# Optimization experiments

Measured on AMD Instinct MI355X. Metric: run time of the kernel, lower is better.

The kernel has to match this reference:

```python
import jax, jax.numpy as jnp
import numpy as np

N = 8192
IN_DIM = 256
HIDDEN = 128


def setup_inputs() -> dict:
    key = jax.random.key(0)
    k1, k2 = jax.random.split(key)
    X = jax.random.normal(k1, (N, IN_DIM), dtype=jnp.float32)
    # nn.Linear(in_dim, hidden, bias=False): weight [hidden, in_dim]
    W = jax.random.normal(k2, (HIDDEN, IN_DIM), dtype=jnp.float32) * (1.0 / np.sqrt(IN_DIM))
    return {"X": X, "W": W}


def reference(X, W):
    # Z = X @ W.T : [N, hidden]
    Z = jnp.einsum('ni,hi->nh', X, W)
    # Dense similarity graph: ReLU(Z Z^T), row-normalized
    A = jax.nn.relu(jnp.einsum('nh,mh->nm', Z, Z))  # [N, N]
    A = A / (A.sum(axis=-1, keepdims=True) + 1e-6)
    out = jnp.einsum('nm,mh->nh', A, Z)  # [N, hidden]
    return (out, A)
```

## Files before the change

### kernel.cpp

```cpp
#include <hip/hip_runtime.h>


#define NR 8192
#define KD 256
#define HD 128

typedef short v8s __attribute__((ext_vector_type(8)));
typedef float v4f __attribute__((ext_vector_type(4)));

static __device__ __forceinline__ ushort f2bf(float f) {
    union { float f; unsigned u; } c; c.f = f;
    unsigned u = c.u;
    u += 0x7fffu + ((u >> 16) & 1u);
    return (ushort)(u >> 16);
}
static __device__ __forceinline__ float bf2f(ushort b) {
    union { unsigned u; float f; } c; c.u = ((unsigned)b) << 16; return c.f;
}
static __device__ __forceinline__ unsigned pk2(float a, float b) {
    union { float f; unsigned u; } x, y; x.f = a; y.f = b;
    unsigned ua = x.u + 0x7fffu + ((x.u >> 16) & 1u);
    unsigned ub = y.u + 0x7fffu + ((y.u >> 16) & 1u);
    return (ua >> 16) | (ub & 0xffff0000u);
}

__global__ __launch_bounds__(256) void k_z(const float* __restrict__ X,
                                           const float* __restrict__ W,
                                           ushort* __restrict__ Zb,
                                           ushort* __restrict__ ZbT) {
    __shared__ ushort Xhi[32][264];
    __shared__ ushort Xlo[32][264];
    int tid = threadIdx.x, lane = tid & 63, wave = tid >> 6;
    int lm = lane & 15, lq = lane >> 4;
    int n0 = blockIdx.x * 32;
    int hbase = wave * 32;
    v8s Whi[2][8], Wlo[2][8];
#pragma unroll
    for (int hi = 0; hi < 2; ++hi) {
        const float* wp = W + (hbase + hi * 16 + lm) * KD + lq * 8;
#pragma unroll
        for (int ks = 0; ks < 8; ++ks) {
            float4 w0 = *(const float4*)(wp + ks * 32);
            float4 w1 = *(const float4*)(wp + ks * 32 + 4);
            float wv[8] = {w0.x, w0.y, w0.z, w0.w, w1.x, w1.y, w1.z, w1.w};
#pragma unroll
            for (int j = 0; j < 8; ++j) {
                ushort h = f2bf(wv[j]);
                Whi[hi][ks][j] = (short)h;
                Wlo[hi][ks][j] = (short)f2bf(wv[j] - bf2f(h));
            }
        }
    }
#pragma unroll
    for (int t = 0; t < 8; ++t) {
        int idx = tid + t * 256;
        int r = idx >> 6, c4 = (idx & 63) * 4;
        float4 x = *(const float4*)(X + (size_t)(n0 + r) * KD + c4);
        ushort h0 = f2bf(x.x), h1 = f2bf(x.y), h2 = f2bf(x.z), h3 = f2bf(x.w);
        unsigned a = ((unsigned)h0) | ((unsigned)h1 << 16);
        unsigned b = ((unsigned)h2) | ((unsigned)h3 << 16);
        unsigned c = ((unsigned)f2bf(x.x - bf2f(h0))) | ((unsigned)f2bf(x.y - bf2f(h1)) << 16);
        unsigned d = ((unsigned)f2bf(x.z - bf2f(h2))) | ((unsigned)f2bf(x.w - bf2f(h3)) << 16);
        *(uint2*)&Xhi[r][c4] = make_uint2(a, b);
        *(uint2*)&Xlo[r][c4] = make_uint2(c, d);
    }
    __syncthreads();
#pragma unroll
    for (int ni = 0; ni < 2; ++ni) {
        v8s Ah[8], Al[8];
#pragma unroll
        for (int ks = 0; ks < 8; ++ks) {
            Ah[ks] = *(const v8s*)&Xhi[ni * 16 + lm][ks * 32 + lq * 8];
            Al[ks] = *(const v8s*)&Xlo[ni * 16 + lm][ks * 32 + lq * 8];
        }
        v4f acc[2] = {{0.f, 0.f, 0.f, 0.f}, {0.f, 0.f, 0.f, 0.f}};
#pragma unroll
        for (int ks = 0; ks < 8; ++ks)
#pragma unroll
            for (int hi = 0; hi < 2; ++hi) {
                acc[hi] = __builtin_amdgcn_mfma_f32_16x16x32_bf16(Ah[ks], Whi[hi][ks], acc[hi], 0, 0, 0);
                acc[hi] = __builtin_amdgcn_mfma_f32_16x16x32_bf16(Ah[ks], Wlo[hi][ks], acc[hi], 0, 0, 0);
                acc[hi] = __builtin_amdgcn_mfma_f32_16x16x32_bf16(Al[ks], Whi[hi][ks], acc[hi], 0, 0, 0);
            }
#pragma unroll
        for (int hi = 0; hi < 2; ++hi) {
            int h = hbase + hi * 16 + lm;
            int nb = n0 + ni * 16 + lq * 4;
            ushort b0 = f2bf(acc[hi][0]), b1 = f2bf(acc[hi][1]);
            ushort b2 = f2bf(acc[hi][2]), b3 = f2bf(acc[hi][3]);
            Zb[(size_t)(nb + 0) * HD + h] = b0;
            Zb[(size_t)(nb + 1) * HD + h] = b1;
            Zb[(size_t)(nb + 2) * HD + h] = b2;
            Zb[(size_t)(nb + 3) * HD + h] = b3;
            *(uint2*)&ZbT[(size_t)h * NR + nb] =
                make_uint2(((unsigned)b0) | ((unsigned)b1 << 16), ((unsigned)b2) | ((unsigned)b3 << 16));
        }
    }
}

__global__ __launch_bounds__(256) void k_rowsum(const ushort* __restrict__ Zb,
                                                float* __restrict__ rowsum) {
    __shared__ ushort ZR[128][136];
    __shared__ ushort ZC[128][136];
    int tid = threadIdx.x, lane = tid & 63, wave = tid >> 6;
    int lm = lane & 15, lq = lane >> 4;
    int rb = blockIdx.x >> 3, cs = blockIdx.x & 7;
    int row0 = rb * 128, cstart = cs * 1024;
#pragma unroll
    for (int t = 0; t < 8; ++t) {
        int idx = tid + t * 256;
        int r = idx >> 4, c8 = (idx & 15) * 8;
        *(uint4*)&ZR[r][c8] = *(const uint4*)(Zb + (size_t)(row0 + r) * HD + c8);
    }
    __syncthreads();
    int wr2 = wave >> 1, wc2 = wave & 1;
    v8s Bfr[4][4];
#pragma unroll
    for (int ri = 0; ri < 4; ++ri)
#pragma unroll
        for (int ks = 0; ks < 4; ++ks)
            Bfr[ri][ks] = *(const v8s*)&ZR[wr2 * 64 + ri * 16 + lm][ks * 32 + lq * 8];
    float rs[4] = {0.f, 0.f, 0.f, 0.f};
    for (int it = 0; it < 8; ++it) {
        int c0 = cstart + it * 128;
        __syncthreads();
#pragma unroll
        for (int t = 0; t < 8; ++t) {
            int idx = tid + t * 256;
            int r = idx >> 4, c8 = (idx & 15) * 8;
            *(uint4*)&ZC[r][c8] = *(const uint4*)(Zb + (size_t)(c0 + r) * HD + c8);
        }
        __syncthreads();
#pragma unroll
        for (int ci = 0; ci < 4; ++ci) {
            v8s Af[4];
#pragma unroll
            for (int ks = 0; ks < 4; ++ks)
                Af[ks] = *(const v8s*)&ZC[wc2 * 64 + ci * 16 + lm][ks * 32 + lq * 8];
            v4f acc[4] = {{0.f,0.f,0.f,0.f},{0.f,0.f,0.f,0.f},{0.f,0.f,0.f,0.f},{0.f,0.f,0.f,0.f}};
#pragma unroll
            for (int ks = 0; ks < 4; ++ks)
#pragma unroll
                for (int ri = 0; ri < 4; ++ri)
                    acc[ri] = __builtin_amdgcn_mfma_f32_16x16x32_bf16(Af[ks], Bfr[ri][ks], acc[ri], 0, 0, 0);
#pragma unroll
            for (int ri = 0; ri < 4; ++ri)
                rs[ri] += fmaxf(acc[ri][0], 0.f) + fmaxf(acc[ri][1], 0.f) +
                          fmaxf(acc[ri][2], 0.f) + fmaxf(acc[ri][3], 0.f);
        }
    }
#pragma unroll
    for (int ri = 0; ri < 4; ++ri) {
        float v = rs[ri];
        v += __shfl_xor(v, 16, 64);
        v += __shfl_xor(v, 32, 64);
        if (lq == 0) atomicAdd(&rowsum[row0 + wr2 * 64 + ri * 16 + lm], v);
    }
}

__global__ __launch_bounds__(256) void k_main(const ushort* __restrict__ Zb,
                                              const ushort* __restrict__ ZbT,
                                              const float* __restrict__ rowsum,
                                              float* __restrict__ outp,
                                              float* __restrict__ Ap) {
    __shared__ ushort ZR[64][136];
    __shared__ ushort ZC[64][136];
    __shared__ ushort ZCT[128][72];
    __shared__ ushort PT[64][72];
    int tid = threadIdx.x, lane = tid & 63, wave = tid >> 6;
    int lm = lane & 15, lq = lane >> 4;
    int rb = blockIdx.x >> 2, cs = blockIdx.x & 3;
    int row0 = rb * 64, colb = cs * 2048;
#pragma unroll
    for (int t = 0; t < 4; ++t) {
        int idx = tid + t * 256;
        int r = idx >> 4, c8 = (idx & 15) * 8;
        *(uint4*)&ZR[r][c8] = *(const uint4*)(Zb + (size_t)(row0 + r) * HD + c8);
    }
    __syncthreads();
    int wr2 = wave >> 1, wc2 = wave & 1;
    v8s Bfr[2][4];
#pragma unroll
    for (int ri = 0; ri < 2; ++ri)
#pragma unroll
        for (int ks = 0; ks < 4; ++ks)
            Bfr[ri][ks] = *(const v8s*)&ZR[wr2 * 32 + ri * 16 + lm][ks * 32 + lq * 8];
    float rsv[2];
#pragma unroll
    for (int ri = 0; ri < 2; ++ri)
        rsv[ri] = 1.0f / (rowsum[row0 + wr2 * 32 + ri * 16 + lm] + 1e-6f);
    v4f U[2][4];
#pragma unroll
    for (int ri = 0; ri < 2; ++ri)
#pragma unroll
        for (int hi = 0; hi < 4; ++hi) U[ri][hi] = (v4f){0.f, 0.f, 0.f, 0.f};

    for (int it = 0; it < 32; ++it) {
        int c0 = colb + it * 64;
        __syncthreads();
#pragma unroll
        for (int t = 0; t < 4; ++t) {
            int idx = tid + t * 256;
            int r = idx >> 4, c8 = (idx & 15) * 8;
            *(uint4*)&ZC[r][c8] = *(const uint4*)(Zb + (size_t)(c0 + r) * HD + c8);
        }
#pragma unroll
        for (int t = 0; t < 4; ++t) {
            int idx = tid + t * 256;
            int hh = idx >> 3, cc8 = (idx & 7) * 8;
            *(uint4*)&ZCT[hh][cc8] = *(const uint4*)(ZbT + (size_t)hh * NR + c0 + cc8);
        }
        __syncthreads();
#pragma unroll
        for (int ci = 0; ci < 2; ++ci) {
            v8s Af[4];
#pragma unroll
            for (int ks = 0; ks < 4; ++ks)
                Af[ks] = *(const v8s*)&ZC[wc2 * 32 + ci * 16 + lm][ks * 32 + lq * 8];
            v4f S0 = {0.f, 0.f, 0.f, 0.f}, S1 = {0.f, 0.f, 0.f, 0.f};
#pragma unroll
            for (int ks = 0; ks < 4; ++ks) {
                S0 = __builtin_amdgcn_mfma_f32_16x16x32_bf16(Af[ks], Bfr[0][ks], S0, 0, 0, 0);
                S1 = __builtin_amdgcn_mfma_f32_16x16x32_bf16(Af[ks], Bfr[1][ks], S1, 0, 0, 0);
            }
            int cb = wc2 * 32 + ci * 16 + lq * 4;
            {
                int r = wr2 * 32 + lm;
                v4f av;
                av[0] = fmaxf(S0[0], 0.f) * rsv[0]; av[1] = fmaxf(S0[1], 0.f) * rsv[0];
                av[2] = fmaxf(S0[2], 0.f) * rsv[0]; av[3] = fmaxf(S0[3], 0.f) * rsv[0];
                __builtin_nontemporal_store(av, (v4f*)(Ap + (size_t)(row0 + r) * NR + c0 + cb));
                *(uint2*)&PT[r][cb] = make_uint2(pk2(av[0], av[1]), pk2(av[2], av[3]));
            }
            {
                int r = wr2 * 32 + 16 + lm;
                v4f av;
                av[0] = fmaxf(S1[0], 0.f) * rsv[1]; av[1] = fmaxf(S1[1], 0.f) * rsv[1];
                av[2] = fmaxf(S1[2], 0.f) * rsv[1]; av[3] = fmaxf(S1[3], 0.f) * rsv[1];
                __builtin_nontemporal_store(av, (v4f*)(Ap + (size_t)(row0 + r) * NR + c0 + cb));
                *(uint2*)&PT[r][cb] = make_uint2(pk2(av[0], av[1]), pk2(av[2], av[3]));
            }
        }
        __syncthreads();
#pragma unroll
        for (int ks = 0; ks < 2; ++ks) {
            v8s P0 = *(const v8s*)&PT[wr2 * 32 + lm][ks * 32 + lq * 8];
            v8s P1 = *(const v8s*)&PT[wr2 * 32 + 16 + lm][ks * 32 + lq * 8];
#pragma unroll
            for (int hi = 0; hi < 4; ++hi) {
                v8s Bz = *(const v8s*)&ZCT[wc2 * 64 + hi * 16 + lm][ks * 32 + lq * 8];
                U[0][hi] = __builtin_amdgcn_mfma_f32_16x16x32_bf16(P0, Bz, U[0][hi], 0, 0, 0);
                U[1][hi] = __builtin_amdgcn_mfma_f32_16x16x32_bf16(P1, Bz, U[1][hi], 0, 0, 0);
            }
        }
    }
#pragma unroll
    for (int ri = 0; ri < 2; ++ri)
#pragma unroll
        for (int hi = 0; hi < 4; ++hi)
#pragma unroll
            for (int j = 0; j < 4; ++j)
                atomicAdd(&outp[(size_t)(row0 + wr2 * 32 + ri * 16 + lq * 4 + j) * HD +
                                wc2 * 64 + hi * 16 + lm],
                          U[ri][hi][j]);
}

extern "C" void kernel_launch(void* const* d_in, const int* in_sizes, int n_in,
                              void* d_out, int out_size, void* d_ws, size_t ws_size,
                              hipStream_t stream) {
    (void)in_sizes; (void)n_in; (void)out_size; (void)ws_size;
    const float* X = (const float*)d_in[0];
    const float* W = (const float*)d_in[1];
    float* outp = (float*)d_out;
    float* Ap = outp + (size_t)NR * HD;
    char* ws = (char*)d_ws;
    ushort* Zb = (ushort*)ws;
    ushort* ZbT = (ushort*)(ws + (size_t)NR * HD * 2);
    float* rowsum = (float*)(ws + (size_t)NR * HD * 4);

    (void)hipMemsetAsync(outp, 0, (size_t)NR * HD * sizeof(float), stream);
    (void)hipMemsetAsync(rowsum, 0, NR * sizeof(float), stream);
    k_z<<<dim3(NR / 32), dim3(256), 0, stream>>>(X, W, Zb, ZbT);
    k_rowsum<<<dim3(512), dim3(256), 0, stream>>>(Zb, rowsum);
    k_main<<<dim3(512), dim3(256), 0, stream>>>(Zb, ZbT, rowsum, outp, Ap);
}
```

Before: 367.1 us.

## Compute unnormalized ReLU(ZZ^T)·Z in rowsum pass, normalize output afterward

The P·Z product is moved out of the A-writing kernel and into the rowsum kernel. It accumulates the unnormalized relu(S)·Z there, and a small final kernel scales the result by the reciprocal row sum. This leaves the A-writing kernel doing only the score GEMM and streaming stores, which may raise its occupancy (launch_bounds 256,4). The cost is more LDS and register pressure in the rowsum kernel (launch_bounds 256,1), an extra workspace buffer with a memset and a pass over it, and bf16 rounding of unnormalized values instead of normalized ones.

```diff
diff --git a/kernel.cpp b/kernel.cpp
--- a/kernel.cpp
+++ b/kernel.cpp
@@ -98,10 +98,14 @@
     }
 }
 
-__global__ __launch_bounds__(256) void k_rowsum(const ushort* __restrict__ Zb,
-                                                float* __restrict__ rowsum) {
+__global__ __launch_bounds__(256, 1) void k_sv(const ushort* __restrict__ Zb,
+                                               const ushort* __restrict__ ZbT,
+                                               float* __restrict__ rowsum,
+                                               float* __restrict__ Vacc) {
     __shared__ ushort ZR[128][136];
     __shared__ ushort ZC[128][136];
+    __shared__ ushort ZCT[128][136];
+    __shared__ ushort PT[128][136];
     int tid = threadIdx.x, lane = tid & 63, wave = tid >> 6;
     int lm = lane & 15, lq = lane >> 4;
     int rb = blockIdx.x >> 3, cs = blockIdx.x & 7;
@@ -121,6 +125,12 @@
         for (int ks = 0; ks < 4; ++ks)
             Bfr[ri][ks] = *(const v8s*)&ZR[wr2 * 64 + ri * 16 + lm][ks * 32 + lq * 8];
     float rs[4] = {0.f, 0.f, 0.f, 0.f};
+    v4f V[4][4];
+#pragma unroll
+    for (int ri = 0; ri < 4; ++ri)
+#pragma unroll
+        for (int hi = 0; hi < 4; ++hi) V[ri][hi] = (v4f){0.f, 0.f, 0.f, 0.f};
+
     for (int it = 0; it < 8; ++it) {
         int c0 = cstart + it * 128;
         __syncthreads();
@@ -130,6 +140,12 @@
             int r = idx >> 4, c8 = (idx & 15) * 8;
             *(uint4*)&ZC[r][c8] = *(const uint4*)(Zb + (size_t)(c0 + r) * HD + c8);
         }
+#pragma unroll
+        for (int t = 0; t < 8; ++t) {
+            int idx = tid + t * 256;
+            int h = idx >> 4, cc8 = (idx & 15) * 8;
+            *(uint4*)&ZCT[h][cc8] = *(const uint4*)(ZbT + (size_t)h * NR + c0 + cc8);
+        }
         __syncthreads();
 #pragma unroll
         for (int ci = 0; ci < 4; ++ci) {
@@ -144,9 +160,28 @@
                 for (int ri = 0; ri < 4; ++ri)
                     acc[ri] = __builtin_amdgcn_mfma_f32_16x16x32_bf16(Af[ks], Bfr[ri][ks], acc[ri], 0, 0, 0);
 #pragma unroll
+            for (int ri = 0; ri < 4; ++ri) {
+                float a0 = fmaxf(acc[ri][0], 0.f), a1 = fmaxf(acc[ri][1], 0.f);
+                float a2 = fmaxf(acc[ri][2], 0.f), a3 = fmaxf(acc[ri][3], 0.f);
+                rs[ri] += a0 + a1 + a2 + a3;
+                *(uint2*)&PT[wr2 * 64 + ri * 16 + lm][wc2 * 64 + ci * 16 + lq * 4] =
+                    make_uint2(pk2(a0, a1), pk2(a2, a3));
+            }
+        }
+        __syncthreads();
+#pragma unroll
+        for (int ks = 0; ks < 4; ++ks) {
+            v8s Pf[4];
+#pragma unroll
             for (int ri = 0; ri < 4; ++ri)
-                rs[ri] += fmaxf(acc[ri][0], 0.f) + fmaxf(acc[ri][1], 0.f) +
-                          fmaxf(acc[ri][2], 0.f) + fmaxf(acc[ri][3], 0.f);
+                Pf[ri] = *(const v8s*)&PT[wr2 * 64 + ri * 16 + lm][ks * 32 + lq * 8];
+#pragma unroll
+            for (int hi = 0; hi < 4; ++hi) {
+                v8s Bz = *(const v8s*)&ZCT[wc2 * 64 + hi * 16 + lm][ks * 32 + lq * 8];
+#pragma unroll
+                for (int ri = 0; ri < 4; ++ri)
+                    V[ri][hi] = __builtin_amdgcn_mfma_f32_16x16x32_bf16(Pf[ri], Bz, V[ri][hi], 0, 0, 0);
+            }
         }
     }
 #pragma unroll
@@ -156,17 +191,22 @@
         v += __shfl_xor(v, 32, 64);
         if (lq == 0) atomicAdd(&rowsum[row0 + wr2 * 64 + ri * 16 + lm], v);
     }
-}
-
-__global__ __launch_bounds__(256) void k_main(const ushort* __restrict__ Zb,
-                                              const ushort* __restrict__ ZbT,
+#pragma unroll
+    for (int ri = 0; ri < 4; ++ri)
+#pragma unroll
+        for (int hi = 0; hi < 4; ++hi)
+#pragma unroll
+            for (int j = 0; j < 4; ++j)
+                atomicAdd(&Vacc[(size_t)(row0 + wr2 * 64 + ri * 16 + lq * 4 + j) * HD +
+                                wc2 * 64 + hi * 16 + lm],
+                          V[ri][hi][j]);
+}
+
+__global__ __launch_bounds__(256, 4) void k_a(const ushort* __restrict__ Zb,
                                               const float* __restrict__ rowsum,
-                                              float* __restrict__ outp,
                                               float* __restrict__ Ap) {
     __shared__ ushort ZR[64][136];
     __shared__ ushort ZC[64][136];
-    __shared__ ushort ZCT[128][72];
-    __shared__ ushort PT[64][72];
     int tid = threadIdx.x, lane = tid & 63, wave = tid >> 6;
     int lm = lane & 15, lq = lane >> 4;
     int rb = blockIdx.x >> 2, cs = blockIdx.x & 3;
@@ -189,11 +229,6 @@
 #pragma unroll
     for (int ri = 0; ri < 2; ++ri)
         rsv[ri] = 1.0f / (rowsum[row0 + wr2 * 32 + ri * 16 + lm] + 1e-6f);
-    v4f U[2][4];
-#pragma unroll
-    for (int ri = 0; ri < 2; ++ri)
-#pragma unroll
-        for (int hi = 0; hi < 4; ++hi) U[ri][hi] = (v4f){0.f, 0.f, 0.f, 0.f};
 
     for (int it = 0; it < 32; ++it) {
         int c0 = colb + it * 64;
@@ -203,12 +238,6 @@
             int idx = tid + t * 256;
             int r = idx >> 4, c8 = (idx & 15) * 8;
             *(uint4*)&ZC[r][c8] = *(const uint4*)(Zb + (size_t)(c0 + r) * HD + c8);
-        }
-#pragma unroll
-        for (int t = 0; t < 4; ++t) {
-            int idx = tid + t * 256;
-            int hh = idx >> 3, cc8 = (idx & 7) * 8;
-            *(uint4*)&ZCT[hh][cc8] = *(const uint4*)(ZbT + (size_t)hh * NR + c0 + cc8);
         }
         __syncthreads();
 #pragma unroll
@@ -230,7 +259,6 @@
                 av[0] = fmaxf(S0[0], 0.f) * rsv[0]; av[1] = fmaxf(S0[1], 0.f) * rsv[0];
                 av[2] = fmaxf(S0[2], 0.f) * rsv[0]; av[3] = fmaxf(S0[3], 0.f) * rsv[0];
                 __builtin_nontemporal_store(av, (v4f*)(Ap + (size_t)(row0 + r) * NR + c0 + cb));
-                *(uint2*)&PT[r][cb] = make_uint2(pk2(av[0], av[1]), pk2(av[2], av[3]));
             }
             {
                 int r = wr2 * 32 + 16 + lm;
@@ -238,31 +266,20 @@
                 av[0] = fmaxf(S1[0], 0.f) * rsv[1]; av[1] = fmaxf(S1[1], 0.f) * rsv[1];
                 av[2] = fmaxf(S1[2], 0.f) * rsv[1]; av[3] = fmaxf(S1[3], 0.f) * rsv[1];
                 __builtin_nontemporal_store(av, (v4f*)(Ap + (size_t)(row0 + r) * NR + c0 + cb));
-                *(uint2*)&PT[r][cb] = make_uint2(pk2(av[0], av[1]), pk2(av[2], av[3]));
-            }
-        }
-        __syncthreads();
-#pragma unroll
-        for (int ks = 0; ks < 2; ++ks) {
-            v8s P0 = *(const v8s*)&PT[wr2 * 32 + lm][ks * 32 + lq * 8];
-            v8s P1 = *(const v8s*)&PT[wr2 * 32 + 16 + lm][ks * 32 + lq * 8];
-#pragma unroll
-            for (int hi = 0; hi < 4; ++hi) {
-                v8s Bz = *(const v8s*)&ZCT[wc2 * 64 + hi * 16 + lm][ks * 32 + lq * 8];
-                U[0][hi] = __builtin_amdgcn_mfma_f32_16x16x32_bf16(P0, Bz, U[0][hi], 0, 0, 0);
-                U[1][hi] = __builtin_amdgcn_mfma_f32_16x16x32_bf16(P1, Bz, U[1][hi], 0, 0, 0);
-            }
-        }
-    }
-#pragma unroll
-    for (int ri = 0; ri < 2; ++ri)
-#pragma unroll
-        for (int hi = 0; hi < 4; ++hi)
-#pragma unroll
-            for (int j = 0; j < 4; ++j)
-                atomicAdd(&outp[(size_t)(row0 + wr2 * 32 + ri * 16 + lq * 4 + j) * HD +
-                                wc2 * 64 + hi * 16 + lm],
-                          U[ri][hi][j]);
+            }
+        }
+    }
+}
+
+__global__ __launch_bounds__(256) void k_out(const float* __restrict__ Vacc,
+                                             const float* __restrict__ rowsum,
+                                             float* __restrict__ outp) {
+    int idx = blockIdx.x * 256 + threadIdx.x;
+    int r = idx >> 5, h4 = (idx & 31) * 4;
+    float rsv = 1.0f / (rowsum[r] + 1e-6f);
+    float4 v = *(const float4*)(Vacc + (size_t)r * HD + h4);
+    float4 o = make_float4(v.x * rsv, v.y * rsv, v.z * rsv, v.w * rsv);
+    *(float4*)(outp + (size_t)r * HD + h4) = o;
 }
 
 extern "C" void kernel_launch(void* const* d_in, const int* in_sizes, int n_in,
@@ -277,10 +294,12 @@
     ushort* Zb = (ushort*)ws;
     ushort* ZbT = (ushort*)(ws + (size_t)NR * HD * 2);
     float* rowsum = (float*)(ws + (size_t)NR * HD * 4);
-
-    (void)hipMemsetAsync(outp, 0, (size_t)NR * HD * sizeof(float), stream);
+    float* Vacc = (float*)(ws + (size_t)NR * HD * 4 + NR * 4);
+
     (void)hipMemsetAsync(rowsum, 0, NR * sizeof(float), stream);
+    (void)hipMemsetAsync(Vacc, 0, (size_t)NR * HD * sizeof(float), stream);
     k_z<<<dim3(NR / 32), dim3(256), 0, stream>>>(X, W, Zb, ZbT);
-    k_rowsum<<<dim3(512), dim3(256), 0, stream>>>(Zb, rowsum);
-    k_main<<<dim3(512), dim3(256), 0, stream>>>(Zb, ZbT, rowsum, outp, Ap);
-}
+    k_sv<<<dim3(512), dim3(256), 0, stream>>>(Zb, ZbT, rowsum, Vacc);
+    k_a<<<dim3(512), dim3(256), 0, stream>>>(Zb, rowsum, Ap);
+    k_out<<<dim3(1024), dim3(256), 0, stream>>>(Vacc, rowsum, outp);
+}
```

New measurement: 446.6 us. 1.22x slower.

## Fuse rowsum with unnormalized A·Z, then write normalized A separately

Applied to the files above, without the earlier changes.

The work is restructured so one kernel computes the row sums and the unnormalized product relu(ZZ^T)·Z together, using split-column partials instead of atomics. A small kernel reduces the partials and applies the normalization to produce the output. A final kernel writes A straight from global/L2 loads without LDS staging, and the P operand now uses the hardware bf16 pack instruction. The partial V buffers are staged in the tail of the A output region, which is overwritten afterwards. This removes the memsets and atomics but computes ZZ^T twice and feeds the PV matmul with unnormalized bf16 values.

```diff
diff --git a/kernel.cpp b/kernel.cpp
--- a/kernel.cpp
+++ b/kernel.cpp
@@ -17,11 +17,10 @@
 static __device__ __forceinline__ float bf2f(ushort b) {
     union { unsigned u; float f; } c; c.u = ((unsigned)b) << 16; return c.f;
 }
-static __device__ __forceinline__ unsigned pk2(float a, float b) {
-    union { float f; unsigned u; } x, y; x.f = a; y.f = b;
-    unsigned ua = x.u + 0x7fffu + ((x.u >> 16) & 1u);
-    unsigned ub = y.u + 0x7fffu + ((y.u >> 16) & 1u);
-    return (ua >> 16) | (ub & 0xffff0000u);
+static __device__ __forceinline__ unsigned cvtpk(float a, float b) {
+    unsigned r;
+    asm("v_cvt_pk_bf16_f32 %0, %1, %2" : "=v"(r) : "v"(a), "v"(b));
+    return r;
 }
 
 __global__ __launch_bounds__(256) void k_z(const float* __restrict__ X,
@@ -98,171 +97,165 @@
     }
 }
 
-__global__ __launch_bounds__(256) void k_rowsum(const ushort* __restrict__ Zb,
-                                                float* __restrict__ rowsum) {
-    __shared__ ushort ZR[128][136];
-    __shared__ ushort ZC[128][136];
+__global__ __launch_bounds__(256) void k_sv(const ushort* __restrict__ Zb,
+                                            const ushort* __restrict__ ZbT,
+                                            float* __restrict__ rsP,
+                                            float* __restrict__ Vp) {
+    __shared__ ushort PT[2][32][136];
+    __shared__ float rsred[4][32];
     int tid = threadIdx.x, lane = tid & 63, wave = tid >> 6;
     int lm = lane & 15, lq = lane >> 4;
-    int rb = blockIdx.x >> 3, cs = blockIdx.x & 7;
-    int row0 = rb * 128, cstart = cs * 1024;
-#pragma unroll
-    for (int t = 0; t < 8; ++t) {
-        int idx = tid + t * 256;
-        int r = idx >> 4, c8 = (idx & 15) * 8;
-        *(uint4*)&ZR[r][c8] = *(const uint4*)(Zb + (size_t)(row0 + r) * HD + c8);
-    }
-    __syncthreads();
-    int wr2 = wave >> 1, wc2 = wave & 1;
-    v8s Bfr[4][4];
-#pragma unroll
-    for (int ri = 0; ri < 4; ++ri)
+    int rb = blockIdx.x >> 2, q = blockIdx.x & 3;
+    int row0 = rb * 32, cbase = q * 2048;
+    v8s Bfr[2][4];
+#pragma unroll
+    for (int ri = 0; ri < 2; ++ri)
 #pragma unroll
         for (int ks = 0; ks < 4; ++ks)
-            Bfr[ri][ks] = *(const v8s*)&ZR[wr2 * 64 + ri * 16 + lm][ks * 32 + lq * 8];
-    float rs[4] = {0.f, 0.f, 0.f, 0.f};
-    for (int it = 0; it < 8; ++it) {
-        int c0 = cstart + it * 128;
+            Bfr[ri][ks] = *(const v8s*)(Zb + (size_t)(row0 + ri * 16 + lm) * HD + ks * 32 + lq * 8);
+    float rs[2] = {0.f, 0.f};
+    v4f V[2][2];
+#pragma unroll
+    for (int ri = 0; ri < 2; ++ri)
+#pragma unroll
+        for (int hi = 0; hi < 2; ++hi) V[ri][hi] = (v4f){0.f, 0.f, 0.f, 0.f};
+
+    const ushort* afp = Zb + (size_t)(cbase + wave * 32 + lm) * HD + lq * 8;
+    const ushort* bzp = ZbT + (size_t)(wave * 32 + lm) * NR + cbase + lq * 8;
+
+    for (int it = 0; it < 16; ++it) {
+        v8s Bz[2][4];
+#pragma unroll
+        for (int hi = 0; hi < 2; ++hi)
+#pragma unroll
+            for (int ks = 0; ks < 4; ++ks)
+                Bz[hi][ks] = *(const v8s*)(bzp + (size_t)hi * 16 * NR + ks * 32);
+#pragma unroll
+        for (int ci = 0; ci < 2; ++ci) {
+            v8s Af[4];
+#pragma unroll
+            for (int ks = 0; ks < 4; ++ks)
+                Af[ks] = *(const v8s*)(afp + (size_t)(ci * 16) * HD + ks * 32);
+            v4f a0 = {0.f, 0.f, 0.f, 0.f}, a1 = {0.f, 0.f, 0.f, 0.f};
+#pragma unroll
+            for (int ks = 0; ks < 4; ++ks) {
+                a0 = __builtin_amdgcn_mfma_f32_16x16x32_bf16(Af[ks], Bfr[0][ks], a0, 0, 0, 0);
+                a1 = __builtin_amdgcn_mfma_f32_16x16x32_bf16(Af[ks], Bfr[1][ks], a1, 0, 0, 0);
+            }
+            int cc = wave * 32 + ci * 16 + lq * 4;
+            {
+                float f0 = fmaxf(a0[0], 0.f), f1 = fmaxf(a0[1], 0.f);
+                float f2 = fmaxf(a0[2], 0.f), f3 = fmaxf(a0[3], 0.f);
+                rs[0] += f0 + f1 + f2 + f3;
+                *(uint2*)&PT[it & 1][lm][cc] = make_uint2(cvtpk(f0, f1), cvtpk(f2, f3));
+            }
+            {
+                float f0 = fmaxf(a1[0], 0.f), f1 = fmaxf(a1[1], 0.f);
+                float f2 = fmaxf(a1[2], 0.f), f3 = fmaxf(a1[3], 0.f);
+                rs[1] += f0 + f1 + f2 + f3;
+                *(uint2*)&PT[it & 1][16 + lm][cc] = make_uint2(cvtpk(f0, f1), cvtpk(f2, f3));
+            }
+        }
         __syncthreads();
 #pragma unroll
-        for (int t = 0; t < 8; ++t) {
-            int idx = tid + t * 256;
-            int r = idx >> 4, c8 = (idx & 15) * 8;
-            *(uint4*)&ZC[r][c8] = *(const uint4*)(Zb + (size_t)(c0 + r) * HD + c8);
-        }
-        __syncthreads();
-#pragma unroll
-        for (int ci = 0; ci < 4; ++ci) {
-            v8s Af[4];
-#pragma unroll
-            for (int ks = 0; ks < 4; ++ks)
-                Af[ks] = *(const v8s*)&ZC[wc2 * 64 + ci * 16 + lm][ks * 32 + lq * 8];
-            v4f acc[4] = {{0.f,0.f,0.f,0.f},{0.f,0.f,0.f,0.f},{0.f,0.f,0.f,0.f},{0.f,0.f,0.f,0.f}};
-#pragma unroll
-            for (int ks = 0; ks < 4; ++ks)
-#pragma unroll
-                for (int ri = 0; ri < 4; ++ri)
-                    acc[ri] = __builtin_amdgcn_mfma_f32_16x16x32_bf16(Af[ks], Bfr[ri][ks], acc[ri], 0, 0, 0);
-#pragma unroll
-            for (int ri = 0; ri < 4; ++ri)
-                rs[ri] += fmaxf(acc[ri][0], 0.f) + fmaxf(acc[ri][1], 0.f) +
-                          fmaxf(acc[ri][2], 0.f) + fmaxf(acc[ri][3], 0.f);
-        }
-    }
-#pragma unroll
-    for (int ri = 0; ri < 4; ++ri) {
+        for (int ks = 0; ks < 4; ++ks) {
+            v8s P0 = *(const v8s*)&PT[it & 1][lm][ks * 32 + lq * 8];
+            v8s P1 = *(const v8s*)&PT[it & 1][16 + lm][ks * 32 + lq * 8];
+#pragma unroll
+            for (int hi = 0; hi < 2; ++hi) {
+                V[0][hi] = __builtin_amdgcn_mfma_f32_16x16x32_bf16(P0, Bz[hi][ks], V[0][hi], 0, 0, 0);
+                V[1][hi] = __builtin_amdgcn_mfma_f32_16x16x32_bf16(P1, Bz[hi][ks], V[1][hi], 0, 0, 0);
+            }
+        }
+        afp += (size_t)128 * HD;
+        bzp += 128;
+    }
+#pragma unroll
+    for (int ri = 0; ri < 2; ++ri) {
         float v = rs[ri];
         v += __shfl_xor(v, 16, 64);
         v += __shfl_xor(v, 32, 64);
-        if (lq == 0) atomicAdd(&rowsum[row0 + wr2 * 64 + ri * 16 + lm], v);
-    }
-}
-
-__global__ __launch_bounds__(256) void k_main(const ushort* __restrict__ Zb,
-                                              const ushort* __restrict__ ZbT,
-                                              const float* __restrict__ rowsum,
-                                              float* __restrict__ outp,
-                                              float* __restrict__ Ap) {
-    __shared__ ushort ZR[64][136];
-    __shared__ ushort ZC[64][136];
-    __shared__ ushort ZCT[128][72];
-    __shared__ ushort PT[64][72];
+        if (lq == 0) rsred[wave][ri * 16 + lm] = v;
+    }
+    __syncthreads();
+    if (tid < 32)
+        rsP[(size_t)q * NR + row0 + tid] =
+            rsred[0][tid] + rsred[1][tid] + rsred[2][tid] + rsred[3][tid];
+    float* vbase = Vp + (size_t)q * NR * HD + (size_t)row0 * HD + wave * 32;
+#pragma unroll
+    for (int ri = 0; ri < 2; ++ri)
+#pragma unroll
+        for (int hi = 0; hi < 2; ++hi)
+#pragma unroll
+            for (int j = 0; j < 4; ++j)
+                vbase[(size_t)(ri * 16 + lq * 4 + j) * HD + hi * 16 + lm] = V[ri][hi][j];
+}
+
+__global__ __launch_bounds__(256) void k_out(const float* __restrict__ Vp,
+                                             const float* __restrict__ rsP,
+                                             float* __restrict__ outp) {
+    int idx = blockIdx.x * 256 + threadIdx.x;
+    int r = idx >> 5, h4 = (idx & 31) * 4;
+    float rsv = 1.0f / (rsP[r] + rsP[NR + r] + rsP[2 * NR + r] + rsP[3 * NR + r] + 1e-6f);
+    size_t o = (size_t)r * HD + h4;
+    float4 v0 = *(const float4*)(Vp + o);
+    float4 v1 = *(const float4*)(Vp + (size_t)NR * HD + o);
+    float4 v2 = *(const float4*)(Vp + 2 * (size_t)NR * HD + o);
+    float4 v3 = *(const float4*)(Vp + 3 * (size_t)NR * HD + o);
+    float4 s = make_float4((v0.x + v1.x + v2.x + v3.x) * rsv, (v0.y + v1.y + v2.y + v3.y) * rsv,
+                           (v0.z + v1.z + v2.z + v3.z) * rsv, (v0.w + v1.w + v2.w + v3.w) * rsv);
+    *(float4*)(outp + o) = s;
+}
+
+__global__ __launch_bounds__(256) void k_a(const ushort* __restrict__ Zb,
+                                           const float* __restrict__ rsP,
+                                           float* __restrict__ Ap) {
     int tid = threadIdx.x, lane = tid & 63, wave = tid >> 6;
     int lm = lane & 15, lq = lane >> 4;
     int rb = blockIdx.x >> 2, cs = blockIdx.x & 3;
     int row0 = rb * 64, colb = cs * 2048;
-#pragma unroll
-    for (int t = 0; t < 4; ++t) {
-        int idx = tid + t * 256;
-        int r = idx >> 4, c8 = (idx & 15) * 8;
-        *(uint4*)&ZR[r][c8] = *(const uint4*)(Zb + (size_t)(row0 + r) * HD + c8);
-    }
-    __syncthreads();
     int wr2 = wave >> 1, wc2 = wave & 1;
     v8s Bfr[2][4];
 #pragma unroll
     for (int ri = 0; ri < 2; ++ri)
 #pragma unroll
         for (int ks = 0; ks < 4; ++ks)
-            Bfr[ri][ks] = *(const v8s*)&ZR[wr2 * 32 + ri * 16 + lm][ks * 32 + lq * 8];
+            Bfr[ri][ks] =
+                *(const v8s*)(Zb + (size_t)(row0 + wr2 * 32 + ri * 16 + lm) * HD + ks * 32 + lq * 8);
     float rsv[2];
 #pragma unroll
-    for (int ri = 0; ri < 2; ++ri)
-        rsv[ri] = 1.0f / (rowsum[row0 + wr2 * 32 + ri * 16 + lm] + 1e-6f);
-    v4f U[2][4];
-#pragma unroll
-    for (int ri = 0; ri < 2; ++ri)
-#pragma unroll
-        for (int hi = 0; hi < 4; ++hi) U[ri][hi] = (v4f){0.f, 0.f, 0.f, 0.f};
-
+    for (int ri = 0; ri < 2; ++ri) {
+        int r = row0 + wr2 * 32 + ri * 16 + lm;
+        rsv[ri] = 1.0f / (rsP[r] + rsP[NR + r] + rsP[2 * NR + r] + rsP[3 * NR + r] + 1e-6f);
+    }
+    const ushort* afp = Zb + (size_t)(colb + wc2 * 32 + lm) * HD + lq * 8;
+    float* ap0 = Ap + (size_t)(row0 + wr2 * 32 + lm) * NR + colb + wc2 * 32 + lq * 4;
+    float* ap1 = ap0 + (size_t)16 * NR;
     for (int it = 0; it < 32; ++it) {
-        int c0 = colb + it * 64;
-        __syncthreads();
-#pragma unroll
-        for (int t = 0; t < 4; ++t) {
-            int idx = tid + t * 256;
-            int r = idx >> 4, c8 = (idx & 15) * 8;
-            *(uint4*)&ZC[r][c8] = *(const uint4*)(Zb + (size_t)(c0 + r) * HD + c8);
-        }
-#pragma unroll
-        for (int t = 0; t < 4; ++t) {
-            int idx = tid + t * 256;
-            int hh = idx >> 3, cc8 = (idx & 7) * 8;
-            *(uint4*)&ZCT[hh][cc8] = *(const uint4*)(ZbT + (size_t)hh * NR + c0 + cc8);
-        }
-        __syncthreads();
 #pragma unroll
         for (int ci = 0; ci < 2; ++ci) {
             v8s Af[4];
 #pragma unroll
             for (int ks = 0; ks < 4; ++ks)
-                Af[ks] = *(const v8s*)&ZC[wc2 * 32 + ci * 16 + lm][ks * 32 + lq * 8];
+                Af[ks] = *(const v8s*)(afp + (size_t)(ci * 16) * HD + ks * 32);
             v4f S0 = {0.f, 0.f, 0.f, 0.f}, S1 = {0.f, 0.f, 0.f, 0.f};
 #pragma unroll
             for (int ks = 0; ks < 4; ++ks) {
                 S0 = __builtin_amdgcn_mfma_f32_16x16x32_bf16(Af[ks], Bfr[0][ks], S0, 0, 0, 0);
                 S1 = __builtin_amdgcn_mfma_f32_16x16x32_bf16(Af[ks], Bfr[1][ks], S1, 0, 0, 0);
             }
-            int cb = wc2 * 32 + ci * 16 + lq * 4;
-            {
-                int r = wr2 * 32 + lm;
-                v4f av;
-                av[0] = fmaxf(S0[0], 0.f) * rsv[0]; av[1] = fmaxf(S0[1], 0.f) * rsv[0];
-                av[2] = fmaxf(S0[2], 0.f) * rsv[0]; av[3] = fmaxf(S0[3], 0.f) * rsv[0];
-                __builtin_nontemporal_store(av, (v4f*)(Ap + (size_t)(row0 + r) * NR + c0 + cb));
-                *(uint2*)&PT[r][cb] = make_uint2(pk2(av[0], av[1]), pk2(av[2], av[3]));
-            }
-            {
-                int r = wr2 * 32 + 16 + lm;
-                v4f av;
-                av[0] = fmaxf(S1[0], 0.f) * rsv[1]; av[1] = fmaxf(S1[1], 0.f) * rsv[1];
-                av[2] = fmaxf(S1[2], 0.f) * rsv[1]; av[3] = fmaxf(S1[3], 0.f) * rsv[1];
-                __builtin_nontemporal_store(av, (v4f*)(Ap + (size_t)(row0 + r) * NR + c0 + cb));
-                *(uint2*)&PT[r][cb] = make_uint2(pk2(av[0], av[1]), pk2(av[2], av[3]));
-            }
-        }
-        __syncthreads();
-#pragma unroll
-        for (int ks = 0; ks < 2; ++ks) {
-            v8s P0 = *(const v8s*)&PT[wr2 * 32 + lm][ks * 32 + lq * 8];
-            v8s P1 = *(const v8s*)&PT[wr2 * 32 + 16 + lm][ks * 32 + lq * 8];
-#pragma unroll
-            for (int hi = 0; hi < 4; ++hi) {
-                v8s Bz = *(const v8s*)&ZCT[wc2 * 64 + hi * 16 + lm][ks * 32 + lq * 8];
-                U[0][hi] = __builtin_amdgcn_mfma_f32_16x16x32_bf16(P0, Bz, U[0][hi], 0, 0, 0);
-                U[1][hi] = __builtin_amdgcn_mfma_f32_16x16x32_bf16(P1, Bz, U[1][hi], 0, 0, 0);
-            }
-        }
-    }
-#pragma unroll
-    for (int ri = 0; ri < 2; ++ri)
-#pragma unroll
-        for (int hi = 0; hi < 4; ++hi)
-#pragma unroll
-            for (int j = 0; j < 4; ++j)
-                atomicAdd(&outp[(size_t)(row0 + wr2 * 32 + ri * 16 + lq * 4 + j) * HD +
-                                wc2 * 64 + hi * 16 + lm],
-                          U[ri][hi][j]);
+            v4f av;
+            av[0] = fmaxf(S0[0], 0.f) * rsv[0]; av[1] = fmaxf(S0[1], 0.f) * rsv[0];
+            av[2] = fmaxf(S0[2], 0.f) * rsv[0]; av[3] = fmaxf(S0[3], 0.f) * rsv[0];
+            __builtin_nontemporal_store(av, (v4f*)(ap0 + ci * 16));
+            av[0] = fmaxf(S1[0], 0.f) * rsv[1]; av[1] = fmaxf(S1[1], 0.f) * rsv[1];
+            av[2] = fmaxf(S1[2], 0.f) * rsv[1]; av[3] = fmaxf(S1[3], 0.f) * rsv[1];
+            __builtin_nontemporal_store(av, (v4f*)(ap1 + ci * 16));
+        }
+        afp += (size_t)64 * HD;
+        ap0 += 64;
+        ap1 += 64;
+    }
 }
 
 extern "C" void kernel_launch(void* const* d_in, const int* in_sizes, int n_in,
@@ -273,14 +266,14 @@
     const float* W = (const float*)d_in[1];
     float* outp = (float*)d_out;
     float* Ap = outp + (size_t)NR * HD;
+    float* Vp = Ap + ((size_t)NR * NR - 4 * (size_t)NR * HD);
     char* ws = (char*)d_ws;
     ushort* Zb = (ushort*)ws;
     ushort* ZbT = (ushort*)(ws + (size_t)NR * HD * 2);
-    float* rowsum = (float*)(ws + (size_t)NR * HD * 4);
-
-    (void)hipMemsetAsync(outp, 0, (size_t)NR * HD * sizeof(float), stream);
-    (void)hipMemsetAsync(rowsum, 0, NR * sizeof(float), stream);
+    float* rsP = (float*)(ws + (size_t)NR * HD * 4);
+
     k_z<<<dim3(NR / 32), dim3(256), 0, stream>>>(X, W, Zb, ZbT);
-    k_rowsum<<<dim3(512), dim3(256), 0, stream>>>(Zb, rowsum);
-    k_main<<<dim3(512), dim3(256), 0, stream>>>(Zb, ZbT, rowsum, outp, Ap);
-}
+    k_sv<<<dim3(1024), dim3(256), 0, stream>>>(Zb, ZbT, rsP, Vp);
+    k_out<<<dim3(1024), dim3(256), 0, stream>>>(Vp, rsP, outp);
+    k_a<<<dim3(512), dim3(256), 0, stream>>>(Zb, rsP, Ap);
+}
```

Result: slower. 483.8 us (+31.8%).

## Fuse rowsum into unnormalized P@Z pass, defer normalization, write A separately

Applied to the files above, without the earlier changes.

The separate rowsum kernel is removed. A new kernel computes ReLU(ZZ^T) once, accumulating both the row sums and the unnormalized product with Z into a workspace buffer. A small kernel then divides by the row sums, and a third kernel recomputes the similarity tile to write the normalized A matrix. The A write is decoupled from the PV pass so that pass avoids the 256MB store, at the cost of recomputing the Z Z^T tiles and adding two launches.

```diff
diff --git a/kernel.cpp b/kernel.cpp
--- a/kernel.cpp
+++ b/kernel.cpp
@@ -98,104 +98,33 @@
     }
 }
 
-__global__ __launch_bounds__(256) void k_rowsum(const ushort* __restrict__ Zb,
-                                                float* __restrict__ rowsum) {
-    __shared__ ushort ZR[128][136];
-    __shared__ ushort ZC[128][136];
-    int tid = threadIdx.x, lane = tid & 63, wave = tid >> 6;
-    int lm = lane & 15, lq = lane >> 4;
-    int rb = blockIdx.x >> 3, cs = blockIdx.x & 7;
-    int row0 = rb * 128, cstart = cs * 1024;
-#pragma unroll
-    for (int t = 0; t < 8; ++t) {
-        int idx = tid + t * 256;
-        int r = idx >> 4, c8 = (idx & 15) * 8;
-        *(uint4*)&ZR[r][c8] = *(const uint4*)(Zb + (size_t)(row0 + r) * HD + c8);
-    }
-    __syncthreads();
-    int wr2 = wave >> 1, wc2 = wave & 1;
-    v8s Bfr[4][4];
-#pragma unroll
-    for (int ri = 0; ri < 4; ++ri)
-#pragma unroll
-        for (int ks = 0; ks < 4; ++ks)
-            Bfr[ri][ks] = *(const v8s*)&ZR[wr2 * 64 + ri * 16 + lm][ks * 32 + lq * 8];
-    float rs[4] = {0.f, 0.f, 0.f, 0.f};
-    for (int it = 0; it < 8; ++it) {
-        int c0 = cstart + it * 128;
-        __syncthreads();
-#pragma unroll
-        for (int t = 0; t < 8; ++t) {
-            int idx = tid + t * 256;
-            int r = idx >> 4, c8 = (idx & 15) * 8;
-            *(uint4*)&ZC[r][c8] = *(const uint4*)(Zb + (size_t)(c0 + r) * HD + c8);
-        }
-        __syncthreads();
-#pragma unroll
-        for (int ci = 0; ci < 4; ++ci) {
-            v8s Af[4];
-#pragma unroll
-            for (int ks = 0; ks < 4; ++ks)
-                Af[ks] = *(const v8s*)&ZC[wc2 * 64 + ci * 16 + lm][ks * 32 + lq * 8];
-            v4f acc[4] = {{0.f,0.f,0.f,0.f},{0.f,0.f,0.f,0.f},{0.f,0.f,0.f,0.f},{0.f,0.f,0.f,0.f}};
-#pragma unroll
-            for (int ks = 0; ks < 4; ++ks)
-#pragma unroll
-                for (int ri = 0; ri < 4; ++ri)
-                    acc[ri] = __builtin_amdgcn_mfma_f32_16x16x32_bf16(Af[ks], Bfr[ri][ks], acc[ri], 0, 0, 0);
-#pragma unroll
-            for (int ri = 0; ri < 4; ++ri)
-                rs[ri] += fmaxf(acc[ri][0], 0.f) + fmaxf(acc[ri][1], 0.f) +
-                          fmaxf(acc[ri][2], 0.f) + fmaxf(acc[ri][3], 0.f);
-        }
-    }
-#pragma unroll
-    for (int ri = 0; ri < 4; ++ri) {
-        float v = rs[ri];
-        v += __shfl_xor(v, 16, 64);
-        v += __shfl_xor(v, 32, 64);
-        if (lq == 0) atomicAdd(&rowsum[row0 + wr2 * 64 + ri * 16 + lm], v);
-    }
-}
-
-__global__ __launch_bounds__(256) void k_main(const ushort* __restrict__ Zb,
-                                              const ushort* __restrict__ ZbT,
-                                              const float* __restrict__ rowsum,
-                                              float* __restrict__ outp,
-                                              float* __restrict__ Ap) {
-    __shared__ ushort ZR[64][136];
+__global__ __launch_bounds__(256) void k_sv(const ushort* __restrict__ Zb,
+                                            const ushort* __restrict__ ZbT,
+                                            float* __restrict__ rowsum,
+                                            float* __restrict__ Vacc) {
     __shared__ ushort ZC[64][136];
     __shared__ ushort ZCT[128][72];
     __shared__ ushort PT[64][72];
     int tid = threadIdx.x, lane = tid & 63, wave = tid >> 6;
     int lm = lane & 15, lq = lane >> 4;
-    int rb = blockIdx.x >> 2, cs = blockIdx.x & 3;
-    int row0 = rb * 64, colb = cs * 2048;
-#pragma unroll
-    for (int t = 0; t < 4; ++t) {
-        int idx = tid + t * 256;
-        int r = idx >> 4, c8 = (idx & 15) * 8;
-        *(uint4*)&ZR[r][c8] = *(const uint4*)(Zb + (size_t)(row0 + r) * HD + c8);
-    }
-    __syncthreads();
+    int rb = blockIdx.x >> 3, cs = blockIdx.x & 7;
+    int row0 = rb * 64, colb = cs * 1024;
     int wr2 = wave >> 1, wc2 = wave & 1;
     v8s Bfr[2][4];
 #pragma unroll
     for (int ri = 0; ri < 2; ++ri)
 #pragma unroll
         for (int ks = 0; ks < 4; ++ks)
-            Bfr[ri][ks] = *(const v8s*)&ZR[wr2 * 32 + ri * 16 + lm][ks * 32 + lq * 8];
-    float rsv[2];
-#pragma unroll
-    for (int ri = 0; ri < 2; ++ri)
-        rsv[ri] = 1.0f / (rowsum[row0 + wr2 * 32 + ri * 16 + lm] + 1e-6f);
+            Bfr[ri][ks] =
+                *(const v8s*)(Zb + (size_t)(row0 + wr2 * 32 + ri * 16 + lm) * HD + ks * 32 + lq * 8);
+    float rs[2] = {0.f, 0.f};
     v4f U[2][4];
 #pragma unroll
     for (int ri = 0; ri < 2; ++ri)
 #pragma unroll
         for (int hi = 0; hi < 4; ++hi) U[ri][hi] = (v4f){0.f, 0.f, 0.f, 0.f};
 
-    for (int it = 0; it < 32; ++it) {
+    for (int it = 0; it < 16; ++it) {
         int c0 = colb + it * 64;
         __syncthreads();
 #pragma unroll
@@ -225,20 +154,16 @@
             }
             int cb = wc2 * 32 + ci * 16 + lq * 4;
             {
-                int r = wr2 * 32 + lm;
-                v4f av;
-                av[0] = fmaxf(S0[0], 0.f) * rsv[0]; av[1] = fmaxf(S0[1], 0.f) * rsv[0];
-                av[2] = fmaxf(S0[2], 0.f) * rsv[0]; av[3] = fmaxf(S0[3], 0.f) * rsv[0];
-                __builtin_nontemporal_store(av, (v4f*)(Ap + (size_t)(row0 + r) * NR + c0 + cb));
-                *(uint2*)&PT[r][cb] = make_uint2(pk2(av[0], av[1]), pk2(av[2], av[3]));
+                float f0 = fmaxf(S0[0], 0.f), f1 = fmaxf(S0[1], 0.f);
+                float f2 = fmaxf(S0[2], 0.f), f3 = fmaxf(S0[3], 0.f);
+                rs[0] += f0 + f1 + f2 + f3;
+                *(uint2*)&PT[wr2 * 32 + lm][cb] = make_uint2(pk2(f0, f1), pk2(f2, f3));
             }
             {
-                int r = wr2 * 32 + 16 + lm;
-                v4f av;
-                av[0] = fmaxf(S1[0], 0.f) * rsv[1]; av[1] = fmaxf(S1[1], 0.f) * rsv[1];
-                av[2] = fmaxf(S1[2], 0.f) * rsv[1]; av[3] = fmaxf(S1[3], 0.f) * rsv[1];
-                __builtin_nontemporal_store(av, (v4f*)(Ap + (size_t)(row0 + r) * NR + c0 + cb));
-                *(uint2*)&PT[r][cb] = make_uint2(pk2(av[0], av[1]), pk2(av[2], av[3]));
+                float f0 = fmaxf(S1[0], 0.f), f1 = fmaxf(S1[1], 0.f);
+                float f2 = fmaxf(S1[2], 0.f), f3 = fmaxf(S1[3], 0.f);
+                rs[1] += f0 + f1 + f2 + f3;
+                *(uint2*)&PT[wr2 * 32 + 16 + lm][cb] = make_uint2(pk2(f0, f1), pk2(f2, f3));
             }
         }
         __syncthreads();
@@ -255,14 +180,90 @@
         }
     }
 #pragma unroll
+    for (int ri = 0; ri < 2; ++ri) {
+        float v = rs[ri];
+        v += __shfl_xor(v, 16, 64);
+        v += __shfl_xor(v, 32, 64);
+        if (lq == 0) atomicAdd(&rowsum[row0 + wr2 * 32 + ri * 16 + lm], v);
+    }
+#pragma unroll
     for (int ri = 0; ri < 2; ++ri)
 #pragma unroll
         for (int hi = 0; hi < 4; ++hi)
 #pragma unroll
             for (int j = 0; j < 4; ++j)
-                atomicAdd(&outp[(size_t)(row0 + wr2 * 32 + ri * 16 + lq * 4 + j) * HD +
+                atomicAdd(&Vacc[(size_t)(row0 + wr2 * 32 + ri * 16 + lq * 4 + j) * HD +
                                 wc2 * 64 + hi * 16 + lm],
                           U[ri][hi][j]);
+}
+
+__global__ __launch_bounds__(256) void k_out(const float* __restrict__ Vacc,
+                                             const float* __restrict__ rowsum,
+                                             float* __restrict__ outp) {
+    int idx = blockIdx.x * 256 + threadIdx.x;
+    int r = idx >> 5, h4 = (idx & 31) * 4;
+    float rsv = 1.0f / (rowsum[r] + 1e-6f);
+    float4 v = *(const float4*)(Vacc + (size_t)r * HD + h4);
+    float4 o = make_float4(v.x * rsv, v.y * rsv, v.z * rsv, v.w * rsv);
+    *(float4*)(outp + (size_t)r * HD + h4) = o;
+}
+
+__global__ __launch_bounds__(256) void k_a(const ushort* __restrict__ Zb,
+                                           const float* __restrict__ rowsum,
+                                           float* __restrict__ Ap) {
+    __shared__ ushort ZC[64][136];
+    int tid = threadIdx.x, lane = tid & 63, wave = tid >> 6;
+    int lm = lane & 15, lq = lane >> 4;
+    int rb = blockIdx.x >> 3, cs = blockIdx.x & 7;
+    int row0 = rb * 64, colb = cs * 1024;
+    int wr2 = wave >> 1, wc2 = wave & 1;
+    v8s Bfr[2][4];
+#pragma unroll
+    for (int ri = 0; ri < 2; ++ri)
+#pragma unroll
+        for (int ks = 0; ks < 4; ++ks)
+            Bfr[ri][ks] =
+                *(const v8s*)(Zb + (size_t)(row0 + wr2 * 32 + ri * 16 + lm) * HD + ks * 32 + lq * 8);
+    float rsv[2];
+#pragma unroll
+    for (int ri = 0; ri < 2; ++ri)
+        rsv[ri] = 1.0f / (rowsum[row0 + wr2 * 32 + ri * 16 + lm] + 1e-6f);
+    float* ap0 = Ap + (size_t)(row0 + wr2 * 32 + lm) * NR + colb + wc2 * 32 + lq * 4;
+    float* ap1 = ap0 + (size_t)16 * NR;
+
+    for (int it = 0; it < 16; ++it) {
+        int c0 = colb + it * 64;
+        __syncthreads();
+#pragma unroll
+        for (int t = 0; t < 4; ++t) {
+            int idx = tid + t * 256;
+            int r = idx >> 4, c8 = (idx & 15) * 8;
+            *(uint4*)&ZC[r][c8] = *(const uint4*)(Zb + (size_t)(c0 + r) * HD + c8);
+        }
+        __syncthreads();
+#pragma unroll
+        for (int ci = 0; ci < 2; ++ci) {
+            v8s Af[4];
+#pragma unroll
+            for (int ks = 0; ks < 4; ++ks)
+                Af[ks] = *(const v8s*)&ZC[wc2 * 32 + ci * 16 + lm][ks * 32 + lq * 8];
+            v4f S0 = {0.f, 0.f, 0.f, 0.f}, S1 = {0.f, 0.f, 0.f, 0.f};
+#pragma unroll
+            for (int ks = 0; ks < 4; ++ks) {
+                S0 = __builtin_amdgcn_mfma_f32_16x16x32_bf16(Af[ks], Bfr[0][ks], S0, 0, 0, 0);
+                S1 = __builtin_amdgcn_mfma_f32_16x16x32_bf16(Af[ks], Bfr[1][ks], S1, 0, 0, 0);
+            }
+            v4f av;
+            av[0] = fmaxf(S0[0], 0.f) * rsv[0]; av[1] = fmaxf(S0[1], 0.f) * rsv[0];
+            av[2] = fmaxf(S0[2], 0.f) * rsv[0]; av[3] = fmaxf(S0[3], 0.f) * rsv[0];
+            __builtin_nontemporal_store(av, (v4f*)(ap0 + ci * 16));
+            av[0] = fmaxf(S1[0], 0.f) * rsv[1]; av[1] = fmaxf(S1[1], 0.f) * rsv[1];
+            av[2] = fmaxf(S1[2], 0.f) * rsv[1]; av[3] = fmaxf(S1[3], 0.f) * rsv[1];
+            __builtin_nontemporal_store(av, (v4f*)(ap1 + ci * 16));
+        }
+        ap0 += 64;
+        ap1 += 64;
+    }
 }
 
 extern "C" void kernel_launch(void* const* d_in, const int* in_sizes, int n_in,
@@ -277,10 +278,12 @@
     ushort* Zb = (ushort*)ws;
     ushort* ZbT = (ushort*)(ws + (size_t)NR * HD * 2);
     float* rowsum = (float*)(ws + (size_t)NR * HD * 4);
-
-    (void)hipMemsetAsync(outp, 0, (size_t)NR * HD * sizeof(float), stream);
+    float* Vacc = (float*)(ws + (size_t)NR * HD * 4 + NR * 4);
+
     (void)hipMemsetAsync(rowsum, 0, NR * sizeof(float), stream);
+    (void)hipMemsetAsync(Vacc, 0, (size_t)NR * HD * sizeof(float), stream);
     k_z<<<dim3(NR / 32), dim3(256), 0, stream>>>(X, W, Zb, ZbT);
-    k_rowsum<<<dim3(512), dim3(256), 0, stream>>>(Zb, rowsum);
-    k_main<<<dim3(512), dim3(256), 0, stream>>>(Zb, ZbT, rowsum, outp, Ap);
-}
+    k_sv<<<dim3(1024), dim3(256), 0, stream>>>(Zb, ZbT, rowsum, Vacc);
+    k_out<<<dim3(1024), dim3(256), 0, stream>>>(Vacc, rowsum, outp);
+    k_a<<<dim3(1024), dim3(256), 0, stream>>>(Zb, rowsum, Ap);
+}
```

After: 431.2 us. 17.5% more time.
